# Performance work log

Hardware: AMD Instinct MI355X
Metric: run time of the kernel (lower is better)

## Reference

```python
import jax, jax.numpy as jnp
import numpy as np

N = 4096
NFEAT = 512
NHID = 60
NCLASS = 4


def setup_inputs() -> dict:
    key = jax.random.key(0)
    ks = jax.random.split(key, 12)
    x = jax.random.normal(ks[0], (N, NFEAT), dtype=jnp.float32)
    # sparse-ish binary adjacency (sub_adj), symmetric not required by the module
    sub_adj = (jax.random.uniform(ks[1], (N, N)) < 0.002).astype(jnp.float32)
    # P_vec: init to ones (torch.sub in reset_parameters is non-inplace, so it stays ones)
    P_vec = jnp.ones((N * (N + 1) // 2,), dtype=jnp.float32)
    s1 = 1.0 / np.sqrt(NFEAT)
    s2 = 1.0 / np.sqrt(NHID)
    W1 = jax.random.normal(ks[2], (NFEAT, NHID), dtype=jnp.float32) * s1
    b1 = jax.random.normal(ks[3], (NHID,), dtype=jnp.float32) * 0.01
    W2 = jax.random.normal(ks[4], (NHID, NHID), dtype=jnp.float32) * s2
    b2 = jax.random.normal(ks[5], (NHID,), dtype=jnp.float32) * 0.01
    W3 = jax.random.normal(ks[6], (NHID, NHID), dtype=jnp.float32) * s2
    b3 = jax.random.normal(ks[7], (NHID,), dtype=jnp.float32) * 0.01
    lin_w = jax.random.normal(ks[8], (NHID, NCLASS), dtype=jnp.float32) * s2
    lin_b = jax.random.normal(ks[9], (NCLASS,), dtype=jnp.float32) * 0.01
    return {"x": x, "sub_adj": sub_adj, "P_vec": P_vec,
            "W1": W1, "b1": b1, "W2": W2, "b2": b2, "W3": W3, "b3": b3,
            "lin_w": lin_w, "lin_b": lin_b}


def reference(x, sub_adj, P_vec, W1, b1, W2, b2, W3, b3, lin_w, lin_b):
    n = sub_adj.shape[0]
    # scatter P_vec into lower triangle (incl. diagonal), then symmetrize
    il, jl = jnp.tril_indices(n)
    M = jnp.zeros((n, n), dtype=P_vec.dtype).at[il, jl].set(P_vec)
    P_hat_symm = M + M.T - jnp.diag(jnp.diag(M))
    # perturbed adjacency with self-loops
    A_tilde = jax.nn.sigmoid(P_hat_symm) * sub_adj + jnp.eye(n, dtype=P_vec.dtype)
    # degree (column sums, matching python sum(adj)); detached in the original
    d = jax.lax.stop_gradient(jnp.sum(A_tilde, axis=0))
    d_inv_sqrt = jnp.where(d > 0, d ** -0.5, 0.0)  # isinf -> 0
    # D^{-1/2} A D^{-1/2} without materializing diag matrices
    norm_adj = d_inv_sqrt[:, None] * A_tilde * d_inv_sqrt[None, :]
    # 3 GCN layers: spmm(norm_adj, x @ W) + b
    h1 = jax.nn.relu(norm_adj @ (x @ W1) + b1)
    h2 = jax.nn.relu(norm_adj @ (h1 @ W2) + b2)
    h3 = norm_adj @ (h2 @ W3) + b3
    logits = h3 @ lin_w + lin_b  # dropout is identity in eval / p=0
    return jax.nn.log_softmax(logits, axis=1)
```

## Files before the change

kernel.cpp:

```cpp
#include <hip/hip_runtime.h>
#include <math.h>

#define NN 4096
#define NFEAT 512
#define NHID 60
#define NCLASS 4
#define CAP 96
#define GSTRIDE 64
#define QCAP 128
#define SCANBLK (NN * NN / 4 / 2048)
#define XWBLK (NN / 4)

__device__ __forceinline__ void scan_f4(const float4 av4, int f4idx,
                                        const float* __restrict__ P,
                                        float* __restrict__ dcol,
                                        int* __restrict__ cnt,
                                        int* __restrict__ cols,
                                        float* __restrict__ vals) {
    const float av[4] = {av4.x, av4.y, av4.z, av4.w};
    const int e0 = f4idx * 4;
    #pragma unroll
    for (int q = 0; q < 4; ++q) {
        if (av[q] != 0.f) {
            const int e = e0 + q;
            const int i = e >> 12;
            const int j = e & (NN - 1);
            const int hi = i > j ? i : j;
            const int lo = i > j ? j : i;
            const float pv = P[((hi * (hi + 1)) >> 1) + lo];
            const float s = av[q] / (1.f + __expf(-pv));
            atomicAdd(&dcol[j], s);
            const int pos = atomicAdd(&cnt[i], 1);
            if (pos < CAP) { cols[i * CAP + pos] = j; vals[i * CAP + pos] = s; }
        }
    }
}

__global__ __launch_bounds__(256) void k_scan_xw(const float* __restrict__ x,
                                                 const float* __restrict__ adj,
                                                 const float* __restrict__ P,
                                                 const float* __restrict__ W1,
                                                 float* __restrict__ dcol,
                                                 int* __restrict__ cnt,
                                                 int* __restrict__ cols,
                                                 float* __restrict__ vals,
                                                 float* __restrict__ g1) {
    __shared__ float xs[4 * NFEAT];
    __shared__ int wq[4][QCAP];
    __shared__ int wq_n[4];
    const int tid = threadIdx.x;
    const int w = tid >> 6, lane = tid & 63;

    if (blockIdx.x < SCANBLK) {
        if (tid < 4) wq_n[tid] = 0;
        __syncthreads();
        const int base = blockIdx.x * 2048 + tid;
        const uint4* adj4 = (const uint4*)adj;
        uint4 a[8];
        #pragma unroll
        for (int u = 0; u < 8; ++u) a[u] = adj4[base + u * 256];
        #pragma unroll
        for (int u = 0; u < 8; ++u) {
            if (a[u].x | a[u].y | a[u].z | a[u].w) {
                const int p = atomicAdd(&wq_n[w], 1);
                if (p < QCAP) wq[w][p] = base + u * 256;
                else {
                    const uint4 v = a[u];
                    const float4 f = make_float4(__uint_as_float(v.x), __uint_as_float(v.y),
                                                 __uint_as_float(v.z), __uint_as_float(v.w));
                    scan_f4(f, base + u * 256, P, dcol, cnt, cols, vals);
                }
            }
        }
        __syncthreads();
        const int n = min(wq_n[w], QCAP);
        for (int l = lane; l < n; l += 64) {
            const int idx = wq[w][l];
            scan_f4(((const float4*)adj)[idx], idx, P, dcol, cnt, cols, vals);
        }
        return;
    }

    const int row0 = (blockIdx.x - SCANBLK) * 4;
    const float4* x4 = (const float4*)x + row0 * (NFEAT / 4);
    float4* xs4 = (float4*)xs;
    xs4[tid]       = x4[tid];
    xs4[tid + 256] = x4[tid + 256];
    __syncthreads();
    const int c = lane < NHID ? lane : 0;
    const float* xrow = xs + w * NFEAT;
    float a0 = 0.f, a1 = 0.f, a2 = 0.f, a3 = 0.f;
    #pragma unroll 4
    for (int k = 0; k < NFEAT; k += 4) {
        a0 = fmaf(xrow[k + 0], W1[(k + 0) * NHID + c], a0);
        a1 = fmaf(xrow[k + 1], W1[(k + 1) * NHID + c], a1);
        a2 = fmaf(xrow[k + 2], W1[(k + 2) * NHID + c], a2);
        a3 = fmaf(xrow[k + 3], W1[(k + 3) * NHID + c], a3);
    }
    g1[(row0 + w) * GSTRIDE + lane] = (lane < NHID) ? (a0 + a1) + (a2 + a3) : 0.f;
}

__device__ __forceinline__ float spmm_row(const float* __restrict__ gin,
                                          const float* __restrict__ dcol,
                                          const int* __restrict__ cnt,
                                          const int* __restrict__ cols,
                                          const float* __restrict__ vals,
                                          int i, int lane, float di) {
    const int nn = min(cnt[i], CAP);
    float acc = gin[i * GSTRIDE + lane] * di;
    const int4*   c4 = (const int4*)(cols + i * CAP);
    const float4* v4 = (const float4*)(vals + i * CAP);
    int e = 0;
    for (; e + 4 <= nn; e += 4) {
        const int4   jj = c4[e >> 2];
        const float4 vv = v4[e >> 2];
        const float f0 = vv.x * rsqrtf(1.f + dcol[jj.x]);
        const float f1 = vv.y * rsqrtf(1.f + dcol[jj.y]);
        const float f2 = vv.z * rsqrtf(1.f + dcol[jj.z]);
        const float f3 = vv.w * rsqrtf(1.f + dcol[jj.w]);
        const float g0 = gin[jj.x * GSTRIDE + lane];
        const float g1 = gin[jj.y * GSTRIDE + lane];
        const float g2 = gin[jj.z * GSTRIDE + lane];
        const float g3 = gin[jj.w * GSTRIDE + lane];
        acc = fmaf(f0, g0, fmaf(f1, g1, fmaf(f2, g2, fmaf(f3, g3, acc))));
    }
    for (; e < nn; ++e) {
        const int j = cols[i * CAP + e];
        const float f = vals[i * CAP + e] * rsqrtf(1.f + dcol[j]);
        acc = fmaf(f, gin[j * GSTRIDE + lane], acc);
    }
    return acc * di;
}

__global__ __launch_bounds__(256) void k_layer(const float* __restrict__ gin,
                                               float* __restrict__ gout,
                                               const float* __restrict__ dcol,
                                               const int* __restrict__ cnt,
                                               const int* __restrict__ cols,
                                               const float* __restrict__ vals,
                                               const float* __restrict__ bias,
                                               const float* __restrict__ W) {
    __shared__ float Ws[NHID * NHID];
    __shared__ float hs[256];
    const int tid = threadIdx.x;
    for (int t = tid; t < NHID * NHID; t += 256) Ws[t] = W[t];
    const int w = tid >> 6, lane = tid & 63;
    const int i = blockIdx.x * 4 + w;
    const float di = rsqrtf(1.f + dcol[i]);
    const float acc = spmm_row(gin, dcol, cnt, cols, vals, i, lane, di);
    hs[w * 64 + lane] = (lane < NHID) ? fmaxf(acc + bias[lane], 0.f) : 0.f;
    __syncthreads();
    const int c = lane < NHID ? lane : 0;
    float o = 0.f;
    #pragma unroll 6
    for (int k = 0; k < NHID; ++k)
        o = fmaf(hs[w * 64 + k], Ws[k * NHID + c], o);
    gout[i * GSTRIDE + lane] = (lane < NHID) ? o : 0.f;
}

__global__ __launch_bounds__(256) void k_final(const float* __restrict__ gin,
                                               float* __restrict__ out,
                                               const float* __restrict__ dcol,
                                               const int* __restrict__ cnt,
                                               const int* __restrict__ cols,
                                               const float* __restrict__ vals,
                                               const float* __restrict__ b3,
                                               const float* __restrict__ lw,
                                               const float* __restrict__ lb) {
    __shared__ float lws[NHID * NCLASS];
    __shared__ float hs[256];
    const int tid = threadIdx.x;
    for (int t = tid; t < NHID * NCLASS; t += 256) lws[t] = lw[t];
    const int w = tid >> 6, lane = tid & 63;
    const int i = blockIdx.x * 4 + w;
    const float di = rsqrtf(1.f + dcol[i]);
    const float acc = spmm_row(gin, dcol, cnt, cols, vals, i, lane, di);
    hs[w * 64 + lane] = (lane < NHID) ? acc + b3[lane] : 0.f;
    __syncthreads();
    if (lane < NCLASS) {
        float o = lb[lane];
        #pragma unroll 4
        for (int k = 0; k < NHID; ++k)
            o = fmaf(hs[w * 64 + k], lws[k * NCLASS + lane], o);
        float m = fmaxf(o, __shfl_xor(o, 1));
        m = fmaxf(m, __shfl_xor(m, 2));
        const float ex = __expf(o - m);
        float ss = ex + __shfl_xor(ex, 1);
        ss += __shfl_xor(ss, 2);
        out[i * NCLASS + lane] = o - m - __logf(ss);
    }
}

extern "C" void kernel_launch(void* const* d_in, const int* in_sizes, int n_in,
                              void* d_out, int out_size, void* d_ws, size_t ws_size,
                              hipStream_t stream) {
    const float* x   = (const float*)d_in[0];
    const float* adj = (const float*)d_in[1];
    const float* P   = (const float*)d_in[2];
    const float* W1  = (const float*)d_in[3];
    const float* b1  = (const float*)d_in[4];
    const float* W2  = (const float*)d_in[5];
    const float* b2  = (const float*)d_in[6];
    const float* W3  = (const float*)d_in[7];
    const float* b3  = (const float*)d_in[8];
    const float* lw  = (const float*)d_in[9];
    const float* lb  = (const float*)d_in[10];
    float* out = (float*)d_out;

    char* ws = (char*)d_ws;
    float* dcol = (float*)(ws);
    int*   cnt  = (int*)(ws + 16384);
    int*   cols = (int*)(ws + 32768);
    float* vals = (float*)(ws + 32768 + 1572864);
    float* bufA = (float*)(ws + 32768 + 2 * 1572864);
    float* bufB = (float*)(ws + 32768 + 2 * 1572864 + 1048576);

    hipMemsetAsync(ws, 0, 32768, stream);

    k_scan_xw<<<SCANBLK + XWBLK, 256, 0, stream>>>(x, adj, P, W1,
                                                   dcol, cnt, cols, vals, bufA);
    k_layer<<<NN / 4, 256, 0, stream>>>(bufA, bufB, dcol, cnt, cols, vals, b1, W2);
    k_layer<<<NN / 4, 256, 0, stream>>>(bufB, bufA, dcol, cnt, cols, vals, b2, W3);
    k_final<<<NN / 4, 256, 0, stream>>>(bufA, out, dcol, cnt, cols, vals, b3, lw, lb);
}
```

Measured before the change: 189.8 us.

## Split adjacency scan into ballot bitmap pass and separate sparse expand kernel

The dense adjacency scan no longer does atomics or builds shared-memory queues. It writes one 64-bit ballot mask per wavefront marking the nonzero float4 chunks. A new kernel walks these bitmap words and re-reads only the marked float4s to compute the sigmoid weights, degree atomics and per-row CSR entries. This removes the divergent per-thread atomic work from the bandwidth-bound scan, at the cost of an extra launch, a 512KB bitmap round trip and a second scattered read of the nonzero chunks.

```diff
diff --git a/kernel.cpp b/kernel.cpp
--- a/kernel.cpp
+++ b/kernel.cpp
@@ -7,9 +7,9 @@
 #define NCLASS 4
 #define CAP 96
 #define GSTRIDE 64
-#define QCAP 128
 #define SCANBLK (NN * NN / 4 / 2048)
 #define XWBLK (NN / 4)
+#define NWORD (NN * NN / 4 / 64)
 
 __device__ __forceinline__ void scan_f4(const float4 av4, int f4idx,
                                         const float* __restrict__ P,
@@ -36,24 +36,16 @@
     }
 }
 
-__global__ __launch_bounds__(256) void k_scan_xw(const float* __restrict__ x,
-                                                 const float* __restrict__ adj,
-                                                 const float* __restrict__ P,
-                                                 const float* __restrict__ W1,
-                                                 float* __restrict__ dcol,
-                                                 int* __restrict__ cnt,
-                                                 int* __restrict__ cols,
-                                                 float* __restrict__ vals,
-                                                 float* __restrict__ g1) {
+__global__ __launch_bounds__(256) void k_bm_xw(const float* __restrict__ x,
+                                               const float* __restrict__ adj,
+                                               const float* __restrict__ W1,
+                                               unsigned long long* __restrict__ bm,
+                                               float* __restrict__ g1) {
     __shared__ float xs[4 * NFEAT];
-    __shared__ int wq[4][QCAP];
-    __shared__ int wq_n[4];
     const int tid = threadIdx.x;
     const int w = tid >> 6, lane = tid & 63;
 
     if (blockIdx.x < SCANBLK) {
-        if (tid < 4) wq_n[tid] = 0;
-        __syncthreads();
         const int base = blockIdx.x * 2048 + tid;
         const uint4* adj4 = (const uint4*)adj;
         uint4 a[8];
@@ -61,22 +53,11 @@
         for (int u = 0; u < 8; ++u) a[u] = adj4[base + u * 256];
         #pragma unroll
         for (int u = 0; u < 8; ++u) {
-            if (a[u].x | a[u].y | a[u].z | a[u].w) {
-                const int p = atomicAdd(&wq_n[w], 1);
-                if (p < QCAP) wq[w][p] = base + u * 256;
-                else {
-                    const uint4 v = a[u];
-                    const float4 f = make_float4(__uint_as_float(v.x), __uint_as_float(v.y),
-                                                 __uint_as_float(v.z), __uint_as_float(v.w));
-                    scan_f4(f, base + u * 256, P, dcol, cnt, cols, vals);
-                }
-            }
-        }
-        __syncthreads();
-        const int n = min(wq_n[w], QCAP);
-        for (int l = lane; l < n; l += 64) {
-            const int idx = wq[w][l];
-            scan_f4(((const float4*)adj)[idx], idx, P, dcol, cnt, cols, vals);
+            const uint4 v = a[u];
+            const bool nz = (v.x | v.y | v.z | v.w) != 0u;
+            const unsigned long long mask = __ballot(nz);
+            if (lane == 0)
+                bm[blockIdx.x * 32 + u * 4 + w] = mask;
         }
         return;
     }
@@ -98,6 +79,23 @@
         a3 = fmaf(xrow[k + 3], W1[(k + 3) * NHID + c], a3);
     }
     g1[(row0 + w) * GSTRIDE + lane] = (lane < NHID) ? (a0 + a1) + (a2 + a3) : 0.f;
+}
+
+__global__ __launch_bounds__(256) void k_expand(const float* __restrict__ adj,
+                                                const float* __restrict__ P,
+                                                const unsigned long long* __restrict__ bm,
+                                                float* __restrict__ dcol,
+                                                int* __restrict__ cnt,
+                                                int* __restrict__ cols,
+                                                float* __restrict__ vals) {
+    const int t = blockIdx.x * 256 + threadIdx.x;
+    unsigned long long word = bm[t];
+    while (word) {
+        const int b = __ffsll((long long)word) - 1;
+        word &= word - 1;
+        const int f4 = t * 64 + b;
+        scan_f4(((const float4*)adj)[f4], f4, P, dcol, cnt, cols, vals);
+    }
 }
 
 __device__ __forceinline__ float spmm_row(const float* __restrict__ gin,
@@ -210,15 +208,16 @@
     char* ws = (char*)d_ws;
     float* dcol = (float*)(ws);
     int*   cnt  = (int*)(ws + 16384);
-    int*   cols = (int*)(ws + 32768);
-    float* vals = (float*)(ws + 32768 + 1572864);
-    float* bufA = (float*)(ws + 32768 + 2 * 1572864);
-    float* bufB = (float*)(ws + 32768 + 2 * 1572864 + 1048576);
+    unsigned long long* bm = (unsigned long long*)(ws + 32768);
+    int*   cols = (int*)(ws + 557056);
+    float* vals = (float*)(ws + 557056 + 1572864);
+    float* bufA = (float*)(ws + 557056 + 2 * 1572864);
+    float* bufB = (float*)(ws + 557056 + 2 * 1572864 + 1048576);
 
     hipMemsetAsync(ws, 0, 32768, stream);
 
-    k_scan_xw<<<SCANBLK + XWBLK, 256, 0, stream>>>(x, adj, P, W1,
-                                                   dcol, cnt, cols, vals, bufA);
+    k_bm_xw<<<SCANBLK + XWBLK, 256, 0, stream>>>(x, adj, W1, bm, bufA);
+    k_expand<<<NWORD / 256, 256, 0, stream>>>(adj, P, bm, dcol, cnt, cols, vals);
     k_layer<<<NN / 4, 256, 0, stream>>>(bufA, bufB, dcol, cnt, cols, vals, b1, W2);
     k_layer<<<NN / 4, 256, 0, stream>>>(bufB, bufA, dcol, cnt, cols, vals, b2, W3);
     k_final<<<NN / 4, 256, 0, stream>>>(bufA, out, dcol, cnt, cols, vals, b3, lw, lb);
```

Result: slower. 197.7 us (+4.1%).
